# Optimization experiments

Measured on AMD Instinct MI355X. Metric: run time of the kernel, lower is better.

The kernel has to match this reference:

```python
import jax, jax.numpy as jnp
from jax import lax
import numpy as np

EPS = 1e-6
LOG_STD_MIN = -20.0
LOG_STD_MAX = 2.0


def _leaky(x):
    return jnp.where(x >= 0, x, 0.01 * x)


def _conv(x, w, b):
    # x: [B,C,H,W], w: [O,C,3,3] -> VALID conv, NCHW
    y = lax.conv_general_dilated(x, w, (1, 1), 'VALID',
                                 dimension_numbers=('NCHW', 'OIHW', 'NCHW'))
    return y + b[None, :, None, None]


def _gru_last(seq, Wih, Whh, bih, bhh):
    # seq: [B,T,In]; PyTorch GRU cell semantics, h0 = 0. Returns h_T: [B,H]
    B = seq.shape[0]
    H = Whh.shape[1]
    h0 = jnp.zeros((B, H), seq.dtype)

    def step(h, x_t):
        gi = x_t @ Wih.T + bih          # [B,3H]
        gh = h @ Whh.T + bhh            # [B,3H]
        i_r, i_z, i_n = jnp.split(gi, 3, axis=-1)
        h_r, h_z, h_n = jnp.split(gh, 3, axis=-1)
        r = jax.nn.sigmoid(i_r + h_r)
        z = jax.nn.sigmoid(i_z + h_z)
        n = jnp.tanh(i_n + r * h_n)
        h_new = (1.0 - z) * n + z * h
        return h_new, None

    h_last, _ = lax.scan(step, h0, jnp.swapaxes(seq, 0, 1))
    return h_last


def setup_inputs() -> dict:
    key = jax.random.key(0)
    ks = jax.random.split(key, 16)
    B, C, T, S = 4096, 3, 64, 128   # batch, in_channels, window, num_stocks
    H = S + 1                        # GRU hidden / action dim = 129
    In = S - 4                       # GRU input size = 124

    def w_init(k, shape, fan_in):
        return jax.random.normal(k, shape, jnp.float32) * np.sqrt(2.0 / fan_in).astype(np.float32)

    inp = {
        'x': jax.random.normal(ks[0], (B, C, T, S), jnp.float32),
        'w': jax.random.uniform(ks[1], (B, H), jnp.float32),
        'eps': jax.random.normal(ks[2], (B, H), jnp.float32),
        'conv1_w': w_init(ks[3], (2 * C, C, 3, 3), C * 9),
        'conv1_b': jnp.zeros((2 * C,), jnp.float32),
        'conv2_w': w_init(ks[4], (1, 2 * C, 3, 3), 2 * C * 9),
        'conv2_b': jnp.zeros((1,), jnp.float32),
        'gru_Wih': w_init(ks[5], (3 * H, In), In),
        'gru_Whh': w_init(ks[6], (3 * H, H), H),
        'gru_bih': jnp.zeros((3 * H,), jnp.float32),
        'gru_bhh': jnp.zeros((3 * H,), jnp.float32),
        'fc_mu_w': w_init(ks[7], (H, 2 * H), 2 * H),
        'fc_mu_b': jnp.zeros((H,), jnp.float32),
        'fc_ls_w': w_init(ks[8], (H, 2 * H), 2 * H),
        'fc_ls_b': jnp.zeros((H,), jnp.float32),
    }
    return inp


def reference(x, w, eps, conv1_w, conv1_b, conv2_w, conv2_b,
              gru_Wih, gru_Whh, gru_bih, gru_bhh,
              fc_mu_w, fc_mu_b, fc_ls_w, fc_ls_b):
    h = _leaky(_conv(x, conv1_w, conv1_b))            # [B,2C,T-2,S-2]
    h = _leaky(_conv(h, conv2_w, conv2_b))            # [B,1,T-4,S-4]
    seq = jnp.squeeze(h, axis=1)                      # [B,T-4,S-4]
    g = _leaky(_gru_last(seq, gru_Wih, gru_Whh, gru_bih, gru_bhh))  # [B,H]
    feat = jnp.concatenate([g, w], axis=-1)           # [B,2H]
    mu = feat @ fc_mu_w.T + fc_mu_b                   # [B,H]
    log_std = jnp.clip(feat @ fc_ls_w.T + fc_ls_b, LOG_STD_MIN, LOG_STD_MAX)
    std = jnp.exp(log_std)
    # Normal.sample() is detached in torch -> stop_gradient
    xs = lax.stop_gradient(mu + std * eps)
    pi_action = jnp.tanh(xs)
    # Normal.log_prob(xs) - log(1 - tanh(xs)^2 + EPS)
    log_pi = (-0.5 * jnp.square((xs - mu) / std) - log_std
              - 0.5 * jnp.log(2.0 * jnp.pi).astype(xs.dtype)
              - jnp.log(1.0 - jnp.square(pi_action) + EPS))
    log_pi = jnp.sum(log_pi, axis=-1, keepdims=True)  # [B,1]
    pi_action = pi_action + 1.0
    pi_action = pi_action / jnp.sum(pi_action, axis=-1, keepdims=True)
    return pi_action, log_pi
```

## Files before the change

kernel.cpp:

```cpp
#include <hip/hip_runtime.h>
#include <math.h>

#define BTOT   4096
#define CIN    3
#define TIN    64
#define SIN    128

#define SEQ_OFF    0
#define G_OFF      (SEQ_OFF + 4096*60*124)
#define HST_OFF    (G_OFF + 4096*129)
#define AWHH_OFF   (HST_OFF + 4096*132)
#define AWIH_OFF   (AWHH_OFF + 64000)
#define MUWP_OFF   (AWIH_OFF + 51200)
#define LSWP_OFF   (MUWP_OFF + 129*260)
#define BUF_OFF    (LSWP_OFF + 129*260)

#define PER_T_GIC   (387 * 4096)
#define PER_T_SBF   655360
#define SBF_T_SH    1310720

typedef __attribute__((ext_vector_type(8))) short bf16x8;
typedef __attribute__((ext_vector_type(4))) float f32x4;

__device__ __forceinline__ float fast_tanh(float x) {
    float ax = fabsf(x);
    float t  = __expf(-2.f * ax);
    float r  = (1.f - t) / (1.f + t);
    return copysignf(r, x);
}
__device__ __forceinline__ float fast_sigmoid(float x) {
    return 1.f / (1.f + __expf(-x));
}
__device__ __forceinline__ unsigned short f2bf(float x) {
    unsigned int u = __float_as_uint(x);
    unsigned int r = u + 0x7FFFu + ((u >> 16) & 1u);
    return (unsigned short)(r >> 16);
}
__device__ __forceinline__ float bf2f(unsigned short b) {
    return __uint_as_float(((unsigned int)b) << 16);
}

__global__ __launch_bounds__(256) void prep_pad(
    const float* __restrict__ Whh, const float* __restrict__ Wih,
    const float* __restrict__ muw, const float* __restrict__ lsw,
    float* __restrict__ ws)
{
    int idx = blockIdx.x * 256 + threadIdx.x;
    const int NHH = 25 * 5 * 2 * 512;
    const int NIA = 25 * 4 * 2 * 512;
    const int N2  = 129 * 260;
    if (idx < NHH) {
        int a      = idx;
        int frag   = a >> 9;
        int within = a & 511;
        int l      = within >> 3;
        int c      = within & 7;
        int half   = frag & 1;
        int q      = frag >> 1;
        int kt     = q % 5;
        int jt     = q / 5;
        int j      = jt * 16 + (l & 15);
        int k      = kt * 32 + (l >> 4) * 8 + c;
        float v    = (j < 387 && k < 129) ? Whh[(size_t)j * 129 + k] : 0.f;
        unsigned short hb = f2bf(v);
        ((short*)(ws + AWHH_OFF))[a] = (short)((half == 0) ? hb : f2bf(v - bf2f(hb)));
    } else if (idx < NHH + NIA) {
        int a      = idx - NHH;
        int frag   = a >> 9;
        int within = a & 511;
        int l      = within >> 3;
        int c      = within & 7;
        int half   = frag & 1;
        int q      = frag >> 1;
        int kt     = q & 3;
        int jt     = q >> 2;
        int j      = jt * 16 + (l & 15);
        int k      = kt * 32 + (l >> 4) * 8 + c;
        float v    = (j < 387 && k < 124) ? Wih[(size_t)j * 124 + k] : 0.f;
        unsigned short hb = f2bf(v);
        ((short*)(ws + AWIH_OFF))[a] = (short)((half == 0) ? hb : f2bf(v - bf2f(hb)));
    } else if (idx < NHH + NIA + N2) {
        int i = idx - NHH - NIA; int j = i / 260, k = i - j * 260;
        ws[MUWP_OFF + i] = (k < 258) ? muw[j * 258 + k] : 0.f;
    } else if (idx < NHH + NIA + 2 * N2) {
        int i = idx - NHH - NIA - N2; int j = i / 260, k = i - j * 260;
        ws[LSWP_OFF + i] = (k < 258) ? lsw[j * 258 + k] : 0.f;
    }
}

#define RACC(F4_, F2_, W0_, W1_, W2_) \
    acc0 += (F4_).x*(W0_) + (F4_).y*(W1_) + (F4_).z*(W2_); \
    acc1 += (F4_).y*(W0_) + (F4_).z*(W1_) + (F4_).w*(W2_); \
    acc2 += (F4_).z*(W0_) + (F4_).w*(W1_) + (F2_).x*(W2_); \
    acc3 += (F4_).w*(W0_) + (F2_).x*(W1_) + (F2_).y*(W2_);

#define LDSET(S, TR_) { \
    S##0_4 = *(const float4*)(xc0 + (TR_) * 128 + s0); \
    S##0_2 = *(const float2*)(xc0 + (TR_) * 128 + f2c); \
    S##1_4 = *(const float4*)(xc1 + (TR_) * 128 + s0); \
    S##1_2 = *(const float2*)(xc1 + (TR_) * 128 + f2c); \
    S##2_4 = *(const float4*)(xc2 + (TR_) * 128 + s0); \
    S##2_2 = *(const float2*)(xc2 + (TR_) * 128 + f2c); }

#define C1STEP(SA, SB, SC, TQ_) { \
    float acc0 = bo, acc1 = bo, acc2 = bo, acc3 = bo; \
    RACC(SA##0_4, SA##0_2, w000, w001, w002) \
    RACC(SA##1_4, SA##1_2, w100, w101, w102) \
    RACC(SA##2_4, SA##2_2, w200, w201, w202) \
    RACC(SB##0_4, SB##0_2, w010, w011, w012) \
    RACC(SB##1_4, SB##1_2, w110, w111, w112) \
    RACC(SB##2_4, SB##2_2, w210, w211, w212) \
    RACC(SC##0_4, SC##0_2, w020, w021, w022) \
    RACC(SC##1_4, SC##1_2, w120, w121, w122) \
    RACC(SC##2_4, SC##2_2, w220, w221, w222) \
    float4 r_; \
    r_.x = (acc0 >= 0.f) ? acc0 : 0.01f * acc0; \
    r_.y = (acc1 >= 0.f) ? acc1 : 0.01f * acc1; \
    r_.z = (acc2 >= 0.f) ? acc2 : 0.01f * acc2; \
    r_.w = (acc3 >= 0.f) ? acc3 : 0.01f * acc3; \
    *(float4*)(h1t + (o * 12 + (TQ_)) * 128 + s0) = r_; }

#define C2SEG(o_, kt_, W0_, W1_, W2_) { \
    const float* rp_ = h1t + ((o_) * 12 + tq + (kt_)) * 128 + s0; \
    float4 v4_ = *(const float4*)rp_; \
    float2 v2_ = *(const float2*)(rp_ + 4); \
    acc0 += v4_.x*(W0_) + v4_.y*(W1_) + v4_.z*(W2_); \
    acc1 += v4_.y*(W0_) + v4_.z*(W1_) + v4_.w*(W2_); \
    acc2 += v4_.z*(W0_) + v4_.w*(W1_) + v2_.x*(W2_); \
    acc3 += v4_.w*(W0_) + v2_.x*(W1_) + v2_.y*(W2_); }

__global__ __launch_bounds__(256) void conv_fused(
    const float* __restrict__ x,
    const float* __restrict__ w1, const float* __restrict__ b1,
    const float* __restrict__ w2, const float* __restrict__ b2,
    float* __restrict__ seq)
{
    __shared__ __attribute__((aligned(16))) float h1t[6 * 12 * 128];
    __shared__ float w1s[162];
    __shared__ float w2s[54];
    __shared__ float b1s[6];
    __shared__ float b2s;

    const int tid  = threadIdx.x;
    const int tile = blockIdx.x;
    const int bb   = blockIdx.y;
    const int T0   = tile * 10;

    if (tid < 162)                  w1s[tid] = w1[tid];
    if (tid >= 192 && tid < 246)    w2s[tid - 192] = w2[tid - 192];
    if (tid >= 248 && tid < 254)    b1s[tid - 248] = b1[tid - 248];
    if (tid == 255)                 b2s = b2[0];
    __syncthreads();

    if (tid < 192) {
        const int o   = tid >> 5;
        const int s0  = (tid & 31) * 4;
        const int f2c = (s0 < 124) ? (s0 + 4) : 122;
        const float* wb = w1s + o * 27;
        float w000 = wb[0],  w001 = wb[1],  w002 = wb[2];
        float w010 = wb[3],  w011 = wb[4],  w012 = wb[5];
        float w020 = wb[6],  w021 = wb[7],  w022 = wb[8];
        float w100 = wb[9],  w101 = wb[10], w102 = wb[11];
        float w110 = wb[12], w111 = wb[13], w112 = wb[14];
        float w120 = wb[15], w121 = wb[16], w122 = wb[17];
        float w200 = wb[18], w201 = wb[19], w202 = wb[20];
        float w210 = wb[21], w211 = wb[22], w212 = wb[23];
        float w220 = wb[24], w221 = wb[25], w222 = wb[26];
        float bo = b1s[o];

        const float* xc0 = x + (size_t)bb * (3 * 64 * 128) + (size_t)T0 * 128;
        const float* xc1 = xc0 + 64 * 128;
        const float* xc2 = xc0 + 2 * 64 * 128;

        float4 A0_4, A1_4, A2_4, B0_4, B1_4, B2_4, C0_4, C1_4, C2_4;
        float2 A0_2, A1_2, A2_2, B0_2, B1_2, B2_2, C0_2, C1_2, C2_2;

        LDSET(A, 0)
        LDSET(B, 1)
        LDSET(C, 2)  C1STEP(A, B, C, 0)
        LDSET(A, 3)  C1STEP(B, C, A, 1)
        LDSET(B, 4)  C1STEP(C, A, B, 2)
        LDSET(C, 5)  C1STEP(A, B, C, 3)
        LDSET(A, 6)  C1STEP(B, C, A, 4)
        LDSET(B, 7)  C1STEP(C, A, B, 5)
        LDSET(C, 8)  C1STEP(A, B, C, 6)
        LDSET(A, 9)  C1STEP(B, C, A, 7)
        LDSET(B, 10) C1STEP(C, A, B, 8)
        LDSET(C, 11) C1STEP(A, B, C, 9)
        LDSET(A, 12) C1STEP(B, C, A, 10)
        LDSET(B, 13) C1STEP(C, A, B, 11)
    }
    __syncthreads();

    {
        float u000 = w2s[0],  u001 = w2s[1],  u002 = w2s[2];
        float u010 = w2s[3],  u011 = w2s[4],  u012 = w2s[5];
        float u020 = w2s[6],  u021 = w2s[7],  u022 = w2s[8];
        float u100 = w2s[9],  u101 = w2s[10], u102 = w2s[11];
        float u110 = w2s[12], u111 = w2s[13], u112 = w2s[14];
        float u120 = w2s[15], u121 = w2s[16], u122 = w2s[17];
        float u200 = w2s[18], u201 = w2s[19], u202 = w2s[20];
        float u210 = w2s[21], u211 = w2s[22], u212 = w2s[23];
        float u220 = w2s[24], u221 = w2s[25], u222 = w2s[26];
        float u300 = w2s[27], u301 = w2s[28], u302 = w2s[29];
        float u310 = w2s[30], u311 = w2s[31], u312 = w2s[32];
        float u320 = w2s[33], u321 = w2s[34], u322 = w2s[35];
        float u400 = w2s[36], u401 = w2s[37], u402 = w2s[38];
        float u410 = w2s[39], u411 = w2s[40], u412 = w2s[41];
        float u420 = w2s[42], u421 = w2s[43], u422 = w2s[44];
        float u500 = w2s[45], u501 = w2s[46], u502 = w2s[47];
        float u510 = w2s[48], u511 = w2s[49], u512 = w2s[50];
        float u520 = w2s[51], u521 = w2s[52], u522 = w2s[53];
        float bo2 = b2s;
        for (int idx = tid; idx < 310; idx += 256) {
            const int tq = idx / 31;
            const int s0 = (idx - tq * 31) * 4;
            float acc0 = bo2, acc1 = bo2, acc2 = bo2, acc3 = bo2;
            C2SEG(0, 0, u000, u001, u002)
            C2SEG(0, 1, u010, u011, u012)
            C2SEG(0, 2, u020, u021, u022)
            C2SEG(1, 0, u100, u101, u102)
            C2SEG(1, 1, u110, u111, u112)
            C2SEG(1, 2, u120, u121, u122)
            C2SEG(2, 0, u200, u201, u202)
            C2SEG(2, 1, u210, u211, u212)
            C2SEG(2, 2, u220, u221, u222)
            C2SEG(3, 0, u300, u301, u302)
            C2SEG(3, 1, u310, u311, u312)
            C2SEG(3, 2, u320, u321, u322)
            C2SEG(4, 0, u400, u401, u402)
            C2SEG(4, 1, u410, u411, u412)
            C2SEG(4, 2, u420, u421, u422)
            C2SEG(5, 0, u500, u501, u502)
            C2SEG(5, 1, u510, u511, u512)
            C2SEG(5, 2, u520, u521, u522)
            float4 r;
            r.x = (acc0 >= 0.f) ? acc0 : 0.01f * acc0;
            r.y = (acc1 >= 0.f) ? acc1 : 0.01f * acc1;
            r.z = (acc2 >= 0.f) ? acc2 : 0.01f * acc2;
            r.w = (acc3 >= 0.f) ? acc3 : 0.01f * acc3;
            *(float4*)(seq + ((size_t)bb * 60 + T0 + tq) * 124 + s0) = r;
        }
    }
}

__global__ __launch_bounds__(256) void seq2bf(
    const float* __restrict__ seq, unsigned long long* __restrict__ sbf,
    int t0, int nt)
{
    long a = (long)blockIdx.x * 256 + threadIdx.x;
    if (a >= (long)nt * 327680) return;
    int tt  = (int)(a / 327680);
    int u   = (int)(a - (long)tt * 327680);
    int chunk = u / 10240;
    int q   = u - chunk * 10240;
    int c0  = (q & 1) * 4;  q >>= 1;
    int ksub = q % 5;       q /= 5;
    int bi  = q & 127;
    int frag = q >> 7;
    int half = frag & 1;
    int kt   = frag >> 1;
    int k0   = kt * 32 + ksub * 8 + c0;

    unsigned long long outp = 0ull;
    if (ksub < 4 && k0 < 124) {
        float4 v = *(const float4*)(seq +
            ((size_t)(chunk * 128 + bi) * 60 + (t0 + tt)) * 124 + k0);
        unsigned short s0, s1, s2, s3;
        if (half == 0) {
            s0 = f2bf(v.x); s1 = f2bf(v.y); s2 = f2bf(v.z); s3 = f2bf(v.w);
        } else {
            s0 = f2bf(v.x - bf2f(f2bf(v.x)));
            s1 = f2bf(v.y - bf2f(f2bf(v.y)));
            s2 = f2bf(v.z - bf2f(f2bf(v.z)));
            s3 = f2bf(v.w - bf2f(f2bf(v.w)));
        }
        outp = (unsigned long long)s0 | ((unsigned long long)s1 << 16)
             | ((unsigned long long)s2 << 32) | ((unsigned long long)s3 << 48);
    }
    sbf[a] = outp;
}

__global__ __launch_bounds__(512) void gi_mfma(
    const short* __restrict__ sbf, const short* __restrict__ awih,
    float* __restrict__ gic, int nt)
{
    const int tid = threadIdx.x;
    const int l   = tid & 63;
    const int w   = tid >> 6;
    const int jt  = blockIdx.y;
    const int bx  = blockIdx.x;
    const int b0  = bx * 128;

    const bf16x8* at = (const bf16x8*)awih;
    const int abase = jt * 8 * 64 + l;
    bf16x8 Ah0 = at[abase + 0 * 128];
    bf16x8 Al0 = at[abase + 0 * 128 + 64];
    bf16x8 Ah1 = at[abase + 1 * 128];
    bf16x8 Al1 = at[abase + 1 * 128 + 64];
    bf16x8 Ah2 = at[abase + 2 * 128];
    bf16x8 Al2 = at[abase + 2 * 128 + 64];
    bf16x8 Ah3 = at[abase + 3 * 128];
    bf16x8 Al3 = at[abase + 3 * 128 + 64];

    const int bn   = w * 16 + (l & 15);
    const int ksub = l >> 4;
    const int off0 = bx * 40960 + (bn * 5 + ksub) * 8;
    const int row0 = ksub * 4;

    for (int tt = 0; tt < nt; ++tt) {
        const short* sb = sbf + (size_t)tt * SBF_T_SH + off0;
        f32x4 acc = {0.f, 0.f, 0.f, 0.f};
        #define GI_KT(KT, AH, AL) { \
            bf16x8 bh = *(const bf16x8*)(sb + ((KT) * 2 + 0) * 5120); \
            bf16x8 bl = *(const bf16x8*)(sb + ((KT) * 2 + 1) * 5120); \
            acc = __builtin_amdgcn_mfma_f32_16x16x32_bf16(AL, bh, acc, 0, 0, 0); \
            acc = __builtin_amdgcn_mfma_f32_16x16x32_bf16(AH, bl, acc, 0, 0, 0); \
            acc = __builtin_amdgcn_mfma_f32_16x16x32_bf16(AH, bh, acc, 0, 0, 0); }
        GI_KT(0, Ah0, Al0)
        GI_KT(1, Ah1, Al1)
        GI_KT(2, Ah2, Al2)
        GI_KT(3, Ah3, Al3)
        #undef GI_KT

        float* gt = gic + (size_t)tt * 387 * 4096;
        #pragma unroll
        for (int i = 0; i < 4; ++i) {
            int j = jt * 16 + row0 + i;
            if (j < 387)
                gt[(size_t)j * 4096 + b0 + bn] = acc[i];
        }
    }
}

__global__ __launch_bounds__(1024) void gru_mfma(
    const float* __restrict__ gic, const short* __restrict__ awhh,
    const float* __restrict__ bih, const float* __restrict__ bhh,
    float* __restrict__ hstate, float* __restrict__ g_out,
    int t0, int nt)
{
    __shared__ __attribute__((aligned(16))) short hbf[2 * 16 * 168];
    __shared__ float hs2[16 * 132];
    __shared__ float GHb[16 * 390];
    __shared__ float bihS[387];
    __shared__ float bhhS[387];

    const int tid  = threadIdx.x;
    const int l    = tid & 63;
    const int w    = tid >> 6;
    const int b0   = blockIdx.x * 16;
    const int bcol = l & 15;
    const int krow = l >> 4;
    const bool has1 = (w < 9);

    if (tid < 387) { bihS[tid] = bih[tid]; bhhS[tid] = bhh[tid]; }
    for (int e = tid; e < 2688; e += 1024) ((unsigned int*)hbf)[e] = 0u;
    if (t0 == 0) {
        for (int e = tid; e < 16 * 132; e += 1024) hs2[e] = 0.f;
        __syncthreads();
    } else {
        for (int e = tid; e < 16 * 132; e += 1024) hs2[e] = hstate[(size_t)b0 * 132 + e];
        __syncthreads();
        for (int e = tid; e < 2064; e += 1024) {
            int r = e & 15, j = e >> 4;
            float v = hs2[r * 132 + j];
            unsigned short hb = f2bf(v);
            hbf[r * 168 + j]        = (short)hb;
            hbf[2688 + r * 168 + j] = (short)f2bf(v - bf2f(hb));
        }
        __syncthreads();
    }

    const bf16x8* at = (const bf16x8*)awhh;

    #define GATE(E, PGA, PGB, PGC) { \
        int r_ = (E) & 15, j_ = (E) >> 4; \
        float pr_  = (PGA) + GHb[r_ * 390 + j_]       + bihS[j_]       + bhhS[j_]; \
        float pz_  = (PGB) + GHb[r_ * 390 + 129 + j_] + bihS[129 + j_] + bhhS[129 + j_]; \
        float gin_ = (PGC) + bihS[258 + j_]; \
        float ghn_ = GHb[r_ * 390 + 258 + j_] + bhhS[258 + j_]; \
        float rg_ = fast_sigmoid(pr_); \
        float zg_ = fast_sigmoid(pz_); \
        float nn_ = fast_tanh(gin_ + rg_ * ghn_); \
        float hn_ = (1.f - zg_) * nn_ + zg_ * hs2[r_ * 132 + j_]; \
        hs2[r_ * 132 + j_] = hn_; \
        unsigned short hb_ = f2bf(hn_); \
        hbf[r_ * 168 + j_]        = (short)hb_; \
        hbf[2688 + r_ * 168 + j_] = (short)f2bf(hn_ - bf2f(hb_)); }

    for (int tt = 0; tt < nt; ++tt) {
        const float* gib = gic + (size_t)tt * 387 * 4096 + b0;
        float pa0, pb0, pc0, pa1, pb1, pc1;
        {
            int r = tid & 15, j = tid >> 4;
            pa0 = gib[(size_t)j * 4096 + r];
            pb0 = gib[(size_t)(129 + j) * 4096 + r];
            pc0 = gib[(size_t)(258 + j) * 4096 + r];
            int e = tid + 1024; r = e & 15; j = e >> 4;
            pa1 = gib[(size_t)j * 4096 + r];
            pb1 = gib[(size_t)(129 + j) * 4096 + r];
            pc1 = gib[(size_t)(258 + j) * 4096 + r];
        }

        f32x4 acc0 = {0.f,0.f,0.f,0.f}, acc1 = {0.f,0.f,0.f,0.f};
        #pragma unroll
        for (int kt = 0; kt < 5; ++kt) {
            bf16x8 bh = *(const bf16x8*)(hbf + bcol * 168 + kt * 32 + krow * 8);
            bf16x8 bl = *(const bf16x8*)(hbf + 2688 + bcol * 168 + kt * 32 + krow * 8);
            {
                int fb = ((w * 5 + kt) * 2) * 64 + l;
                bf16x8 Ah = at[fb], Al = at[fb + 64];
                acc0 = __builtin_amdgcn_mfma_f32_16x16x32_bf16(Al, bh, acc0, 0, 0, 0);
                acc0 = __builtin_amdgcn_mfma_f32_16x16x32_bf16(Ah, bl, acc0, 0, 0, 0);
                acc0 = __builtin_amdgcn_mfma_f32_16x16x32_bf16(Ah, bh, acc0, 0, 0, 0);
            }
            if (has1) {
                int fb = (((16 + w) * 5 + kt) * 2) * 64 + l;
                bf16x8 Ah = at[fb], Al = at[fb + 64];
                acc1 = __builtin_amdgcn_mfma_f32_16x16x32_bf16(Al, bh, acc1, 0, 0, 0);
                acc1 = __builtin_amdgcn_mfma_f32_16x16x32_bf16(Ah, bl, acc1, 0, 0, 0);
                acc1 = __builtin_amdgcn_mfma_f32_16x16x32_bf16(Ah, bh, acc1, 0, 0, 0);
            }
        }
        {
            int rb = bcol * 390;
            int j0 = w * 16 + krow * 4;
            GHb[rb + j0 + 0] = acc0[0];
            GHb[rb + j0 + 1] = acc0[1];
            GHb[rb + j0 + 2] = acc0[2];
            GHb[rb + j0 + 3] = acc0[3];
            if (has1) {
                if (w < 8) {
                    int j1 = (16 + w) * 16 + krow * 4;
                    GHb[rb + j1 + 0] = acc1[0];
                    GHb[rb + j1 + 1] = acc1[1];
                    GHb[rb + j1 + 2] = acc1[2];
                    GHb[rb + j1 + 3] = acc1[3];
                } else if (krow == 0) {
                    GHb[rb + 384] = acc1[0];
                    GHb[rb + 385] = acc1[1];
                    GHb[rb + 386] = acc1[2];
                }
            }
        }
        __syncthreads();

        GATE(tid,        pa0, pb0, pc0)
        GATE(tid + 1024, pa1, pb1, pc1)
        if (tid < 16) {
            float ta = gib[(size_t)128 * 4096 + tid];
            float tb = gib[(size_t)257 * 4096 + tid];
            float tc = gib[(size_t)386 * 4096 + tid];
            GATE(2048 + tid, ta, tb, tc)
        }
        __syncthreads();
    }

    for (int e = tid; e < 16 * 132; e += 1024) hstate[(size_t)b0 * 132 + e] = hs2[e];
    if (t0 + nt >= 60) {
        for (int e = tid; e < 2064; e += 1024) {
            int r = e & 15, j = e >> 4;
            float v = hs2[r * 132 + j];
            g_out[(size_t)(b0 + r) * 129 + j] = (v >= 0.f) ? v : 0.01f * v;
        }
        if (tid < 16) {
            float v = hs2[tid * 132 + 128];
            g_out[(size_t)(b0 + tid) * 129 + 128] = (v >= 0.f) ? v : 0.01f * v;
        }
    }
    #undef GATE
}

__global__ __launch_bounds__(256) void head_kernel(
    const float* __restrict__ gbuf, const float* __restrict__ wvec,
    const float* __restrict__ eps,
    const float* __restrict__ muwp, const float* __restrict__ lswp,
    const float* __restrict__ mub,  const float* __restrict__ lsb,
    float* __restrict__ out)
{
    __shared__ __attribute__((aligned(16))) float feat[16 * 260];
    __shared__ float PA[16 * 130];
    __shared__ float TERM[16 * 130];
    __shared__ float ROWSUM[16];
    __shared__ float ROWLOG[16];

    const int tid = threadIdx.x;
    const int b0  = blockIdx.x * 16;

    for (int i = tid; i < 16 * 260; i += 256) {
        int r = i / 260;
        int k = i - r * 260;
        float v = 0.f;
        if (k < 129)       v = gbuf[(size_t)(b0 + r) * 129 + k];
        else if (k < 258)  v = wvec[(size_t)(b0 + r) * 129 + (k - 129)];
        feat[i] = v;
    }
    __syncthreads();

    for (int idx = tid; idx < 16 * 129; idx += 256) {
        int r = idx & 15;
        int j = idx >> 4;
        const float4* fv = (const float4*)(feat + r * 260);
        const float4* mw = (const float4*)(muwp + (size_t)j * 260);
        const float4* lw = (const float4*)(lswp + (size_t)j * 260);
        float am = 0.f, al = 0.f;
        for (int k = 0; k < 65; ++k) {
            float4 f = fv[k];
            float4 m = mw[k];
            float4 l = lw[k];
            am += f.x * m.x + f.y * m.y + f.z * m.z + f.w * m.w;
            al += f.x * l.x + f.y * l.y + f.z * l.z + f.w * l.w;
        }
        float mu = am + mub[j];
        float ls = fminf(fmaxf(al + lsb[j], -20.f), 2.f);
        float sd = __expf(ls);
        float e  = eps[(size_t)(b0 + r) * 129 + j];
        float xv = mu + sd * e;
        float pa = fast_tanh(xv);
        float tt = (xv - mu) / sd;
        float term = -0.5f * tt * tt - ls - 0.91893853320467274f
                     - __logf(1.f - pa * pa + 1e-6f);
        PA[r * 130 + j]   = pa;
        TERM[r * 130 + j] = term;
    }
    __syncthreads();

    {
        int r = tid >> 4;
        int i = tid & 15;
        float sp = 0.f, st = 0.f;
        for (int j = i; j < 129; j += 16) {
            sp += PA[r * 130 + j];
            st += TERM[r * 130 + j];
        }
        for (int off = 8; off > 0; off >>= 1) {
            sp += __shfl_down(sp, off, 16);
            st += __shfl_down(st, off, 16);
        }
        if (i == 0) { ROWSUM[r] = sp + 129.f; ROWLOG[r] = st; }
    }
    __syncthreads();

    for (int idx = tid; idx < 16 * 129; idx += 256) {
        int r = idx & 15;
        int j = idx >> 4;
        out[(size_t)(b0 + r) * 129 + j] = (PA[r * 130 + j] + 1.f) / ROWSUM[r];
    }
    if (tid < 16)
        out[(size_t)4096 * 129 + b0 + tid] = ROWLOG[tid];
}

extern "C" void kernel_launch(void* const* d_in, const int* in_sizes, int n_in,
                              void* d_out, int out_size, void* d_ws, size_t ws_size,
                              hipStream_t stream)
{
    const float* x   = (const float*)d_in[0];
    const float* wv  = (const float*)d_in[1];
    const float* eps = (const float*)d_in[2];
    const float* c1w = (const float*)d_in[3];
    const float* c1b = (const float*)d_in[4];
    const float* c2w = (const float*)d_in[5];
    const float* c2b = (const float*)d_in[6];
    const float* Wih = (const float*)d_in[7];
    const float* Whh = (const float*)d_in[8];
    const float* bih = (const float*)d_in[9];
    const float* bhh = (const float*)d_in[10];
    const float* muw = (const float*)d_in[11];
    const float* mub = (const float*)d_in[12];
    const float* lsw = (const float*)d_in[13];
    const float* lsb = (const float*)d_in[14];

    float* ws     = (float*)d_ws;
    float* seq    = ws + SEQ_OFF;
    float* g      = ws + G_OFF;
    float* hstate = ws + HST_OFF;
    const short* awhh = (const short*)(ws + AWHH_OFF);
    const short* awih = (const short*)(ws + AWIH_OFF);
    float* muwp   = ws + MUWP_OFF;
    float* lswp   = ws + LSWP_OFF;
    float* outp   = (float*)d_out;

    const long per_t = (long)PER_T_GIC + PER_T_SBF;
    long avail = (long)(ws_size / 4) - (long)BUF_OFF;
    int CT = 60;
    if (avail < 60 * per_t) {
        CT = (int)(avail / per_t);
        if (CT < 1) CT = 1;
        if (CT > 60) CT = 60;
    }
    float* sbff = ws + BUF_OFF;
    float* gic  = ws + BUF_OFF + (size_t)CT * PER_T_SBF;

    const int prep_elems = 25 * 5 * 2 * 512 + 25 * 4 * 2 * 512 + 2 * (129 * 260);
    prep_pad<<<(prep_elems + 255) / 256, 256, 0, stream>>>(Whh, Wih, muw, lsw, ws);
    conv_fused<<<dim3(6, BTOT), 256, 0, stream>>>(x, c1w, c1b, c2w, c2b, seq);

    for (int t0 = 0; t0 < 60; t0 += CT) {
        int nt = 60 - t0; if (nt > CT) nt = CT;
        long nb = ((long)nt * 327680 + 255) / 256;
        seq2bf<<<(int)nb, 256, 0, stream>>>(seq, (unsigned long long*)sbff, t0, nt);
        gi_mfma<<<dim3(32, 25), 512, 0, stream>>>((const short*)sbff, awih, gic, nt);
        gru_mfma<<<256, 1024, 0, stream>>>(gic, awhh, bih, bhh, hstate, g, t0, nt);
    }
    head_kernel<<<BTOT / 16, 256, 0, stream>>>(g, wv, eps, muwp, lswp, mub, lsb, outp);
}
```

Baseline: 1.513 ms.

## Fuse bf16 hi/lo split into conv epilogue and drop seq2bf kernel

The conv kernel now writes its output straight into the bf16 hi/lo fragment layout that the input-projection MFMA kernel consumes, so the fp32 seq intermediate and the separate seq2bf conversion pass are gone. A small kernel zeroes the padding slots (k from 124 to 127) that conv never writes. This removes a full fp32 write and re-read of the sequence plus one launch per chunk. In exchange the conv kernel does scattered 8-byte stores, and the whole 60-step sbf buffer must be resident in the workspace.

```diff
diff --git a/kernel.cpp b/kernel.cpp
--- a/kernel.cpp
+++ b/kernel.cpp
@@ -6,17 +6,16 @@
 #define TIN    64
 #define SIN    128
 
-#define SEQ_OFF    0
-#define G_OFF      (SEQ_OFF + 4096*60*124)
+#define G_OFF      0
 #define HST_OFF    (G_OFF + 4096*129)
 #define AWHH_OFF   (HST_OFF + 4096*132)
 #define AWIH_OFF   (AWHH_OFF + 64000)
 #define MUWP_OFF   (AWIH_OFF + 51200)
 #define LSWP_OFF   (MUWP_OFF + 129*260)
-#define BUF_OFF    (LSWP_OFF + 129*260)
+#define SBF_OFF    (LSWP_OFF + 129*260)
+#define GIC_OFF    (SBF_OFF + 60*655360)
 
 #define PER_T_GIC   (387 * 4096)
-#define PER_T_SBF   655360
 #define SBF_T_SH    1310720
 
 typedef __attribute__((ext_vector_type(8))) short bf16x8;
@@ -88,6 +87,19 @@
     }
 }
 
+__global__ __launch_bounds__(256) void sbf_padzero(short* __restrict__ sbf)
+{
+    int a = blockIdx.x * 256 + threadIdx.x;
+    if (a >= 60 * 32 * 128 * 2) return;
+    int half  = a & 1;
+    int bi    = (a >> 1) & 127;
+    int chunk = (a >> 8) & 31;
+    int t     = a >> 13;
+    size_t s = (size_t)t * SBF_T_SH + (size_t)chunk * 40960
+             + (size_t)(6 + half) * 5120 + (size_t)bi * 40 + 3 * 8 + 4;
+    *(unsigned long long*)(sbf + s) = 0ull;
+}
+
 #define RACC(F4_, F2_, W0_, W1_, W2_) \
     acc0 += (F4_).x*(W0_) + (F4_).y*(W1_) + (F4_).z*(W2_); \
     acc1 += (F4_).y*(W0_) + (F4_).z*(W1_) + (F4_).w*(W2_); \
@@ -133,7 +145,7 @@
     const float* __restrict__ x,
     const float* __restrict__ w1, const float* __restrict__ b1,
     const float* __restrict__ w2, const float* __restrict__ b2,
-    float* __restrict__ seq)
+    short* __restrict__ sbf)
 {
     __shared__ __attribute__((aligned(16))) float h1t[6 * 12 * 128];
     __shared__ float w1s[162];
@@ -212,6 +224,8 @@
         float u510 = w2s[48], u511 = w2s[49], u512 = w2s[50];
         float u520 = w2s[51], u521 = w2s[52], u522 = w2s[53];
         float bo2 = b2s;
+        const int chunk = bb >> 7;
+        const int bi    = bb & 127;
         for (int idx = tid; idx < 310; idx += 256) {
             const int tq = idx / 31;
             const int s0 = (idx - tq * 31) * 4;
@@ -234,56 +248,33 @@
             C2SEG(5, 0, u500, u501, u502)
             C2SEG(5, 1, u510, u511, u512)
             C2SEG(5, 2, u520, u521, u522)
-            float4 r;
-            r.x = (acc0 >= 0.f) ? acc0 : 0.01f * acc0;
-            r.y = (acc1 >= 0.f) ? acc1 : 0.01f * acc1;
-            r.z = (acc2 >= 0.f) ? acc2 : 0.01f * acc2;
-            r.w = (acc3 >= 0.f) ? acc3 : 0.01f * acc3;
-            *(float4*)(seq + ((size_t)bb * 60 + T0 + tq) * 124 + s0) = r;
-        }
-    }
-}
-
-__global__ __launch_bounds__(256) void seq2bf(
-    const float* __restrict__ seq, unsigned long long* __restrict__ sbf,
-    int t0, int nt)
-{
-    long a = (long)blockIdx.x * 256 + threadIdx.x;
-    if (a >= (long)nt * 327680) return;
-    int tt  = (int)(a / 327680);
-    int u   = (int)(a - (long)tt * 327680);
-    int chunk = u / 10240;
-    int q   = u - chunk * 10240;
-    int c0  = (q & 1) * 4;  q >>= 1;
-    int ksub = q % 5;       q /= 5;
-    int bi  = q & 127;
-    int frag = q >> 7;
-    int half = frag & 1;
-    int kt   = frag >> 1;
-    int k0   = kt * 32 + ksub * 8 + c0;
-
-    unsigned long long outp = 0ull;
-    if (ksub < 4 && k0 < 124) {
-        float4 v = *(const float4*)(seq +
-            ((size_t)(chunk * 128 + bi) * 60 + (t0 + tt)) * 124 + k0);
-        unsigned short s0, s1, s2, s3;
-        if (half == 0) {
-            s0 = f2bf(v.x); s1 = f2bf(v.y); s2 = f2bf(v.z); s3 = f2bf(v.w);
-        } else {
-            s0 = f2bf(v.x - bf2f(f2bf(v.x)));
-            s1 = f2bf(v.y - bf2f(f2bf(v.y)));
-            s2 = f2bf(v.z - bf2f(f2bf(v.z)));
-            s3 = f2bf(v.w - bf2f(f2bf(v.w)));
-        }
-        outp = (unsigned long long)s0 | ((unsigned long long)s1 << 16)
-             | ((unsigned long long)s2 << 32) | ((unsigned long long)s3 << 48);
-    }
-    sbf[a] = outp;
+            float r0 = (acc0 >= 0.f) ? acc0 : 0.01f * acc0;
+            float r1 = (acc1 >= 0.f) ? acc1 : 0.01f * acc1;
+            float r2 = (acc2 >= 0.f) ? acc2 : 0.01f * acc2;
+            float r3 = (acc3 >= 0.f) ? acc3 : 0.01f * acc3;
+            unsigned short H0 = f2bf(r0), H1 = f2bf(r1), H2 = f2bf(r2), H3 = f2bf(r3);
+            unsigned short Q0 = f2bf(r0 - bf2f(H0));
+            unsigned short Q1 = f2bf(r1 - bf2f(H1));
+            unsigned short Q2 = f2bf(r2 - bf2f(H2));
+            unsigned short Q3 = f2bf(r3 - bf2f(H3));
+            unsigned long long hp = (unsigned long long)H0 | ((unsigned long long)H1 << 16)
+                                  | ((unsigned long long)H2 << 32) | ((unsigned long long)H3 << 48);
+            unsigned long long lp = (unsigned long long)Q0 | ((unsigned long long)Q1 << 16)
+                                  | ((unsigned long long)Q2 << 32) | ((unsigned long long)Q3 << 48);
+            const int kt   = s0 >> 5;
+            const int ksub = (s0 >> 3) & 3;
+            const int c0   = s0 & 7;
+            size_t sb = (size_t)(T0 + tq) * SBF_T_SH + (size_t)chunk * 40960
+                      + (size_t)(kt * 2) * 5120 + (size_t)bi * 40 + ksub * 8 + c0;
+            *(unsigned long long*)(sbf + sb)        = hp;
+            *(unsigned long long*)(sbf + sb + 5120) = lp;
+        }
+    }
 }
 
 __global__ __launch_bounds__(512) void gi_mfma(
     const short* __restrict__ sbf, const short* __restrict__ awih,
-    float* __restrict__ gic, int nt)
+    float* __restrict__ gic, int t0, int nt)
 {
     const int tid = threadIdx.x;
     const int l   = tid & 63;
@@ -309,7 +300,7 @@
     const int row0 = ksub * 4;
 
     for (int tt = 0; tt < nt; ++tt) {
-        const short* sb = sbf + (size_t)tt * SBF_T_SH + off0;
+        const short* sb = sbf + (size_t)(t0 + tt) * SBF_T_SH + off0;
         f32x4 acc = {0.f, 0.f, 0.f, 0.f};
         #define GI_KT(KT, AH, AL) { \
             bf16x8 bh = *(const bf16x8*)(sb + ((KT) * 2 + 0) * 5120); \
@@ -571,35 +562,32 @@
     const float* lsb = (const float*)d_in[14];
 
     float* ws     = (float*)d_ws;
-    float* seq    = ws + SEQ_OFF;
     float* g      = ws + G_OFF;
     float* hstate = ws + HST_OFF;
     const short* awhh = (const short*)(ws + AWHH_OFF);
     const short* awih = (const short*)(ws + AWIH_OFF);
     float* muwp   = ws + MUWP_OFF;
     float* lswp   = ws + LSWP_OFF;
+    short* sbf    = (short*)(ws + SBF_OFF);
+    float* gic    = ws + GIC_OFF;
     float* outp   = (float*)d_out;
 
-    const long per_t = (long)PER_T_GIC + PER_T_SBF;
-    long avail = (long)(ws_size / 4) - (long)BUF_OFF;
+    long avail = (long)(ws_size / 4) - (long)GIC_OFF;
     int CT = 60;
-    if (avail < 60 * per_t) {
-        CT = (int)(avail / per_t);
+    if (avail < 60L * PER_T_GIC) {
+        CT = (int)(avail / PER_T_GIC);
         if (CT < 1) CT = 1;
         if (CT > 60) CT = 60;
     }
-    float* sbff = ws + BUF_OFF;
-    float* gic  = ws + BUF_OFF + (size_t)CT * PER_T_SBF;
 
     const int prep_elems = 25 * 5 * 2 * 512 + 25 * 4 * 2 * 512 + 2 * (129 * 260);
     prep_pad<<<(prep_elems + 255) / 256, 256, 0, stream>>>(Whh, Wih, muw, lsw, ws);
-    conv_fused<<<dim3(6, BTOT), 256, 0, stream>>>(x, c1w, c1b, c2w, c2b, seq);
+    sbf_padzero<<<(60 * 32 * 128 * 2 + 255) / 256, 256, 0, stream>>>(sbf);
+    conv_fused<<<dim3(6, BTOT), 256, 0, stream>>>(x, c1w, c1b, c2w, c2b, sbf);
 
     for (int t0 = 0; t0 < 60; t0 += CT) {
         int nt = 60 - t0; if (nt > CT) nt = CT;
-        long nb = ((long)nt * 327680 + 255) / 256;
-        seq2bf<<<(int)nb, 256, 0, stream>>>(seq, (unsigned long long*)sbff, t0, nt);
-        gi_mfma<<<dim3(32, 25), 512, 0, stream>>>((const short*)sbff, awih, gic, nt);
+        gi_mfma<<<dim3(32, 25), 512, 0, stream>>>(sbf, awih, gic, t0, nt);
         gru_mfma<<<256, 1024, 0, stream>>>(gic, awhh, bih, bhh, hstate, g, t0, nt);
     }
     head_kernel<<<BTOT / 16, 256, 0, stream>>>(g, wv, eps, muwp, lswp, mub, lsb, outp);
```

Result: faster. 1.320 ms (-12.7%).
